# Kernel tuning notes

Hardware: AMD Instinct MI355X
Metric: run time of the kernel (lower is better)

## Reference

```python
import jax, jax.numpy as jnp
import numpy as np

NL = 8  # number of wavenet cells


def _causal_dil_conv(x, w, b, dil):
    # x: (B, Cin, T), w: (Cout, Cin, K) -> (B, Cout, T), left-padded (causal)
    pad = (w.shape[-1] - 1) * dil
    y = jax.lax.conv_general_dilated(
        x, w, window_strides=(1,), padding=[(pad, 0)],
        rhs_dilation=(dil,), dimension_numbers=('NCH', 'OIH', 'NCH'))
    return y + b[None, :, None]


def setup_inputs() -> dict:
    key = jax.random.key(0)
    ks = jax.random.split(key, 12)
    T, B, d_lag, d_cov, d, K = 2048, 16, 1, 7, 256, 2
    s = 0.05
    return {
        'x_lag': jax.random.normal(ks[0], (T, B, d_lag), jnp.float32),
        'x_cov': jax.random.normal(ks[1], (T, B, d_cov), jnp.float32),
        'up_W': jax.random.normal(ks[2], (d_lag + d_cov, d), jnp.float32) * s,
        'up_b': jax.random.normal(ks[3], (d,), jnp.float32) * s,
        'dil_w': jax.random.normal(ks[4], (NL, 2 * d, d, K), jnp.float32) * s,
        'dil_b': jax.random.normal(ks[5], (NL, 2 * d), jnp.float32) * s,
        'skip_w': jax.random.normal(ks[6], (NL, 2 * d, d, 1), jnp.float32) * s,
        'skip_b': jax.random.normal(ks[7], (NL, 2 * d), jnp.float32) * s,
        'loc_W': jax.random.normal(ks[8], (d, 1), jnp.float32) * s,
        'loc_b': jax.random.normal(ks[9], (1,), jnp.float32) * s,
        'proj_W': jax.random.normal(ks[10], (1, 1), jnp.float32) * s,
        'proj_b': jax.random.normal(ks[11], (1,), jnp.float32) * s,
        'd_outputseqlen': 96,
    }


def reference(x_lag, x_cov, up_W, up_b, dil_w, dil_b, skip_w, skip_b,
              loc_W, loc_b, proj_W, proj_b, d_outputseqlen):
    T = x_lag.shape[0]
    h = jnp.concatenate([x_lag, x_cov[:T]], axis=-1)          # (T,B,d_lag+d_cov)
    h = h @ up_W + up_b                                        # (T,B,d)
    h = jnp.transpose(h, (1, 2, 0))                            # (B,d,T)
    skip = jnp.zeros_like(h)
    for i in range(NL):
        z = _causal_dil_conv(h, dil_w[i], dil_b[i], 2 ** i)    # (B,2d,T)
        f, g = jnp.split(z, 2, axis=1)
        gated = jnp.tanh(f) * jax.nn.sigmoid(g)                # (B,d,T)
        z2 = _causal_dil_conv(gated, skip_w[i], skip_b[i], 1)  # (B,2d,T)
        h_next, skip_next = jnp.split(z2, 2, axis=1)
        h = h + h_next
        skip = skip + skip_next
    out = jnp.transpose(skip[:, :, -d_outputseqlen:], (2, 0, 1))  # (L,B,d)
    loc = out @ loc_W + loc_b                                     # (L,B,1)
    y = jnp.transpose(loc, (1, 0, 2))[..., None]                  # (B,L,1,1)
    return y @ proj_W + proj_b                                    # (B,L,1,c_out)
```

## Files before the change

### kernel.cpp

```cpp
#include <hip/hip_runtime.h>
#include <math.h>
#include <stdint.h>

#define T_TOTAL 2048
#define NB 16
#define D 256
#define T0 1696
#define TBUF 352
#define TSKIP 1952
#define LOUT 96

typedef __bf16 bf16x8 __attribute__((ext_vector_type(8)));
typedef __bf16 bf16x4v __attribute__((ext_vector_type(4)));
typedef float f32x4 __attribute__((ext_vector_type(4)));

__device__ __forceinline__ void gload_lds16(const void* src, void* lds_dst) {
    auto g = (const __attribute__((address_space(1))) void*)(uintptr_t)src;
    auto l = (__attribute__((address_space(3))) void*)(uintptr_t)(
                 (uint32_t)(uintptr_t)lds_dst);
    __builtin_amdgcn_global_load_lds(g, l, 16, 0, 0);
}

__device__ __forceinline__ void decode_tile(int id, int gridx, int& rt, int& ct) {
    int k = id & 7;
    int j = id >> 3;
    int rpx = gridx >> 6;
    rt = k * rpx + (j >> 3);
    ct = j & 7;
}

__global__ __launch_bounds__(256) void prep_up(
    const float* __restrict__ dil_w, const float* __restrict__ skip_w,
    const float* __restrict__ x_lag, const float* __restrict__ x_cov,
    const float* __restrict__ up_W, const float* __restrict__ up_b,
    const float* __restrict__ loc_W,
    __bf16* __restrict__ wT, __bf16* __restrict__ w2,
    float* __restrict__ hf, __bf16* __restrict__ hb,
    float* __restrict__ vWp)
{
    const int g0 = blockIdx.x * 256 + threadIdx.x;
    const int NT = 2048 * 256;

    for (int u = g0; u < 8 * 512 * 32; u += NT) {
        int j = u & 31;
        int cog = u >> 5;
        const float* src = dil_w + ((size_t)cog << 9) + (j << 4);
        float4 a = *(const float4*)(src);
        float4 b = *(const float4*)(src + 4);
        float4 c = *(const float4*)(src + 8);
        float4 d = *(const float4*)(src + 12);
        bf16x8 t0 = {(__bf16)a.x, (__bf16)a.z, (__bf16)b.x, (__bf16)b.z,
                     (__bf16)c.x, (__bf16)c.z, (__bf16)d.x, (__bf16)d.z};
        bf16x8 t1 = {(__bf16)a.y, (__bf16)a.w, (__bf16)b.y, (__bf16)b.w,
                     (__bf16)c.y, (__bf16)c.w, (__bf16)d.y, (__bf16)d.w};
        *(bf16x8*)(wT + ((size_t)cog << 9) + (j << 3)) = t0;
        *(bf16x8*)(wT + ((size_t)cog << 9) + 256 + (j << 3)) = t1;
    }
    for (int u = g0; u < 8 * 256 * 32; u += NT) {
        int row = u >> 5, j = u & 31;
        int ly = row >> 8, co = row & 255;
        const float* src = skip_w + (((size_t)(ly << 9) + co) << 8) + (j << 3);
        float4 a = *(const float4*)(src);
        float4 b = *(const float4*)(src + 4);
        bf16x8 v = {(__bf16)a.x, (__bf16)a.y, (__bf16)a.z, (__bf16)a.w,
                    (__bf16)b.x, (__bf16)b.y, (__bf16)b.z, (__bf16)b.w};
        *(bf16x8*)(w2 + ((size_t)row << 8) + (j << 3)) = v;
    }
    for (int u = g0; u < TBUF * NB * D; u += NT) {
        int row = u >> 8, c = u & 255;
        int tt = row >> 4, b = row & 15, t = T0 + tt;
        float acc = up_b[c] + x_lag[t * NB + b] * up_W[c];
        const float* cov = &x_cov[(t * NB + b) * 7];
        #pragma unroll
        for (int j = 0; j < 7; ++j)
            acc += cov[j] * up_W[(j + 1) * D + c];
        hf[u] = acc;
        hb[u] = (__bf16)acc;
    }
    for (int u = g0; u < 16384; u += NT) {
        int part = u >> 11;
        int r = u & 2047;
        int ly = r >> 8, ci = r & 255;
        const float* sw = skip_w + (((size_t)(ly << 9) + 256 + (part << 5)) << 8) + ci;
        float acc = 0.f;
        #pragma unroll 8
        for (int c = 0; c < 32; ++c)
            acc += sw[(size_t)c << 8] * loc_W[(part << 5) + c];
        vWp[u] = acc;
    }
}

__global__ __launch_bounds__(512, 4) void gate_n32(
    const __bf16* __restrict__ hb, __bf16* __restrict__ gated,
    const __bf16* __restrict__ wTl, const float* __restrict__ gbias,
    __bf16* __restrict__ gsv, int do_save,
    int tb, int dil, int M)
{
    __shared__ __align__(16) unsigned char lds[32768];
    int rt, ct;
    decode_tile(blockIdx.x, gridDim.x, rt, ct);
    const int m0 = rt << 6;
    if (m0 >= M) return;
    const int cb = ct << 5;
    const int tid = threadIdx.x;
    const int lane = tid & 63, wid = tid >> 6;
    const int wm = wid >> 1, wn = wid & 1;
    const int l15 = lane & 15, l4 = lane >> 4;
    const int arow = (wid << 3) + (lane >> 3);
    const int ach = lane & 7;
    const int aswz = (ach ^ (arow & 7)) << 3;
    const int bwid = wid & 3, bhalf = wid >> 2;
    const int brow = (bwid << 3) + (lane >> 3);
    const int bswz = (ach ^ (brow & 7)) << 3;
    const int roff1 = (tb - T0) * 16;
    const int roff0 = roff1 - dil * 16;

    f32x4 accf = {}, accg = {};

    auto stage = [&](int t, int buf) {
        const int k0 = t << 6;
        const int ci0 = k0 & 255;
        const int roff = (t < 4) ? roff0 : roff1;
        unsigned char* base = lds + buf * 16384;
        int m = m0 + arow; if (m >= M) m = M - 1;
        gload_lds16(hb + (size_t)(m + roff) * 256 + ci0 + aswz,
                    base + (wid << 10));
        gload_lds16(wTl + (size_t)(cb + bhalf * 256 + brow) * 512 + k0 + bswz,
                    base + 8192 + (bhalf << 12) + (bwid << 10));
    };

    stage(0, 0);
    for (int t = 0; t < 8; ++t) {
        const int buf = t & 1;
        if (t < 7) {
            stage(t + 1, buf ^ 1);
            asm volatile("s_waitcnt vmcnt(2)" ::: "memory");
        } else {
            asm volatile("s_waitcnt vmcnt(0)" ::: "memory");
        }
        __builtin_amdgcn_s_barrier();
        const unsigned char* base = lds + buf * 16384;
        __builtin_amdgcn_s_setprio(1);
        #pragma unroll
        for (int ks = 0; ks < 2; ++ks) {
            const int kb = (ks << 6) + (l4 << 4);
            int r = (wm << 4) + l15;
            bf16x8 av = *(const bf16x8*)(base + r * 128 + (kb ^ ((r & 7) << 4)));
            int n = (wn << 4) + l15;
            int o = n * 128 + (kb ^ ((n & 7) << 4));
            bf16x8 bfv = *(const bf16x8*)(base + 8192 + o);
            bf16x8 bgv = *(const bf16x8*)(base + 12288 + o);
            accf = __builtin_amdgcn_mfma_f32_16x16x32_bf16(av, bfv, accf, 0, 0, 0);
            accg = __builtin_amdgcn_mfma_f32_16x16x32_bf16(av, bgv, accg, 0, 0, 0);
        }
        __builtin_amdgcn_s_setprio(0);
        __builtin_amdgcn_s_barrier();
    }

    {
        const int ms0 = (TSKIP - tb) * 16;
        const int soff = (tb - TSKIP) * 16;
        int c = cb + (wn << 4) + l15;
        float bfb = gbias[c], bgb = gbias[c + 256];
        #pragma unroll
        for (int r = 0; r < 4; ++r) {
            int m = m0 + (wm << 4) + (l4 << 2) + r;
            if (m < M) {
                float fv = accf[r] + bfb;
                float gv = accg[r] + bgb;
                float th = 2.0f / (1.0f + __expf(-2.0f * fv)) - 1.0f;
                float sg = 1.0f / (1.0f + __expf(-gv));
                __bf16 val = (__bf16)(th * sg);
                gated[(size_t)m * 256 + c] = val;
                if (do_save && m >= ms0)
                    gsv[(size_t)(m + soff) * 256 + c] = val;
            }
        }
    }
}

__global__ __launch_bounds__(512, 4) void skip_h(
    const __bf16* __restrict__ gated, const __bf16* __restrict__ w2l,
    float* __restrict__ hf, __bf16* __restrict__ hb,
    const float* __restrict__ sbias, int tb, int M)
{
    __shared__ __align__(16) unsigned char lds[24576];
    int rt, ct;
    decode_tile(blockIdx.x, gridDim.x, rt, ct);
    const int m0 = rt << 6;
    if (m0 >= M) return;
    const int cb = ct << 5;
    const int tid = threadIdx.x;
    const int lane = tid & 63, wid = tid >> 6;
    const int wm = wid >> 1, wn = wid & 1;
    const int l15 = lane & 15, l4 = lane >> 4;
    const int arow = (wid << 3) + (lane >> 3);
    const int ach = lane & 7;
    const int aswz = (ach ^ (arow & 7)) << 3;
    const int brow = (wid << 3) + (lane >> 3);
    const int bswz = (ach ^ (brow & 7)) << 3;
    const int roff1 = (tb - T0) * 16;

    f32x4 acch = {};

    auto stage = [&](int t, int buf) {
        const int k0 = t << 6;
        unsigned char* base = lds + buf * 12288;
        int m = m0 + arow; if (m >= M) m = M - 1;
        gload_lds16(gated + (size_t)m * 256 + k0 + aswz,
                    base + (wid << 10));
        if (wid < 4)
            gload_lds16(w2l + (size_t)(cb + brow) * 256 + k0 + bswz,
                        base + 8192 + (wid << 10));
    };

    stage(0, 0);
    for (int t = 0; t < 4; ++t) {
        const int buf = t & 1;
        if (t < 3) {
            stage(t + 1, buf ^ 1);
            if (wid < 4) { asm volatile("s_waitcnt vmcnt(2)" ::: "memory"); }
            else         { asm volatile("s_waitcnt vmcnt(1)" ::: "memory"); }
        } else {
            asm volatile("s_waitcnt vmcnt(0)" ::: "memory");
        }
        __builtin_amdgcn_s_barrier();
        const unsigned char* base = lds + buf * 12288;
        __builtin_amdgcn_s_setprio(1);
        #pragma unroll
        for (int ks = 0; ks < 2; ++ks) {
            const int kb = (ks << 6) + (l4 << 4);
            int r = (wm << 4) + l15;
            bf16x8 av = *(const bf16x8*)(base + r * 128 + (kb ^ ((r & 7) << 4)));
            int n = (wn << 4) + l15;
            int o = n * 128 + (kb ^ ((n & 7) << 4));
            bf16x8 bhv = *(const bf16x8*)(base + 8192 + o);
            acch = __builtin_amdgcn_mfma_f32_16x16x32_bf16(av, bhv, acch, 0, 0, 0);
        }
        __builtin_amdgcn_s_setprio(0);
        __builtin_amdgcn_s_barrier();
    }

    {
        int c = cb + (wn << 4) + l15;
        float bhb = sbias[c];
        #pragma unroll
        for (int r = 0; r < 4; ++r) {
            int m = m0 + (wm << 4) + (l4 << 2) + r;
            if (m < M) {
                size_t hi = (size_t)(m + roff1) * 256 + c;
                float hv = hf[hi] + acch[r] + bhb;
                hf[hi] = hv;
                hb[hi] = (__bf16)hv;
            }
        }
    }
}

__global__ __launch_bounds__(256) void final_v2(
    const __bf16* __restrict__ gsave, const __bf16* __restrict__ gated,
    const float* __restrict__ vWp, const float* __restrict__ skip_b,
    const float* __restrict__ loc_W, const float* __restrict__ loc_b,
    const float* __restrict__ proj_W, const float* __restrict__ proj_b,
    float* __restrict__ out)
{
    int tid = threadIdx.x;
    int wid = tid >> 6, lane = tid & 63;
    int o = blockIdx.x * 4 + wid;
    float acc = 0.f;
    #pragma unroll
    for (int ly = 0; ly < 8; ++ly) {
        const __bf16* g = (ly < 7) ? gsave + (((size_t)ly * 1536 + o) << 8)
                                   : gated + ((size_t)o << 8);
        bf16x4v gv = *(const bf16x4v*)(g + (lane << 2));
        float4 vw = {0.f, 0.f, 0.f, 0.f};
        #pragma unroll
        for (int p = 0; p < 8; ++p) {
            float4 vp = *(const float4*)(vWp + (p << 11) + (ly << 8) + (lane << 2));
            vw.x += vp.x; vw.y += vp.y; vw.z += vp.z; vw.w += vp.w;
        }
        acc += (float)gv[0] * vw.x + (float)gv[1] * vw.y
             + (float)gv[2] * vw.z + (float)gv[3] * vw.w;
    }
    #pragma unroll
    for (int j = 0; j < 32; ++j) {
        int idx = lane + (j << 6);
        int ly = idx >> 8, c = idx & 255;
        acc += skip_b[(ly << 9) + 256 + c] * loc_W[c];
    }
    #pragma unroll
    for (int off = 32; off; off >>= 1) acc += __shfl_down(acc, off);
    if (lane == 0) {
        int l = o >> 4, b = o & 15;
        out[b * LOUT + l] = (acc + loc_b[0]) * proj_W[0] + proj_b[0];
    }
}

extern "C" void kernel_launch(void* const* d_in, const int* in_sizes, int n_in,
                              void* d_out, int out_size, void* d_ws, size_t ws_size,
                              hipStream_t stream)
{
    const float* x_lag  = (const float*)d_in[0];
    const float* x_cov  = (const float*)d_in[1];
    const float* up_W   = (const float*)d_in[2];
    const float* up_b   = (const float*)d_in[3];
    const float* dil_w  = (const float*)d_in[4];
    const float* dil_b  = (const float*)d_in[5];
    const float* skip_w = (const float*)d_in[6];
    const float* skip_b = (const float*)d_in[7];
    const float* loc_W  = (const float*)d_in[8];
    const float* loc_b  = (const float*)d_in[9];
    const float* proj_W = (const float*)d_in[10];
    const float* proj_b = (const float*)d_in[11];
    float* out = (float*)d_out;

    unsigned char* ws = (unsigned char*)d_ws;
    float*  hf    = (float*)ws;
    __bf16* hb    = (__bf16*)(ws + 5767168);
    __bf16* gated = (__bf16*)(ws + 8650752);
    __bf16* gsave = (__bf16*)(ws + 11534336);
    __bf16* wT    = (__bf16*)(ws + 17039360);
    __bf16* w2    = (__bf16*)(ws + 21233664);
    float*  vWp   = (float*)(ws + 22282240);

    hipLaunchKernelGGL(prep_up, dim3(2048), dim3(256), 0, stream,
                       dil_w, skip_w, x_lag, x_cov, up_W, up_b, loc_W,
                       wT, w2, hf, hb, vWp);

    for (int i = 0; i < 8; ++i) {
        int dil = 1 << i;
        int tb  = T0 + 2 * dil;
        int M   = (T_TOTAL - tb) * NB;
        int mt  = (M + 63) >> 6;
        int mtp = (mt + 7) & ~7;
        const __bf16* wTl = wT + (size_t)i * 512 * 512;
        const __bf16* w2l = w2 + (size_t)i * 256 * 256;
        const float* gb = dil_b + (size_t)i * 512;
        const float* sb = skip_b + (size_t)i * 512;

        hipLaunchKernelGGL(gate_n32, dim3(mtp * 8), dim3(512), 0, stream,
                           hb, gated, wTl, gb,
                           gsave + (size_t)i * 1536 * 256, i < 7 ? 1 : 0,
                           tb, dil, M);
        if (i < 7)
            hipLaunchKernelGGL(skip_h, dim3(mtp * 8), dim3(512), 0, stream,
                               gated, w2l, hf, hb, sb, tb, M);
    }
    hipLaunchKernelGGL(final_v2, dim3(LOUT * NB / 4), dim3(256), 0, stream,
                       gsave, gated, vWp, skip_b, loc_W, loc_b, proj_W, proj_b,
                       out);
}
```

Measured before the change: 123.6 us.

## Fold skip conv into next layer's gate GEMM via precomputed product weights

Precomputes V = W_dil(i+1) · W_skip_h(i) so each layer's gate GEMM reads the previous layer's gated activations directly, using K=1024 instead of waiting for the h update. This lets the skip/h update of layer i run concurrently with the gate of layer i+1 in one fused launch. Double-buffered h and gated buffers avoid read/write hazards, and per-layer tail contributions are accumulated incrementally instead of saved and reduced at the end. It costs a doubled gate GEMM K dimension, an extra prep GEMM, and extra bf16 rounding of the composed weights.

```diff
diff --git a/kernel.cpp b/kernel.cpp
--- a/kernel.cpp
+++ b/kernel.cpp
@@ -34,7 +34,7 @@
     const float* __restrict__ x_lag, const float* __restrict__ x_cov,
     const float* __restrict__ up_W, const float* __restrict__ up_b,
     const float* __restrict__ loc_W,
-    __bf16* __restrict__ wT, __bf16* __restrict__ w2,
+    __bf16* __restrict__ wT, __bf16* __restrict__ w2, __bf16* __restrict__ w2T,
     float* __restrict__ hf, __bf16* __restrict__ hb,
     float* __restrict__ vWp)
 {
@@ -56,7 +56,7 @@
         *(bf16x8*)(wT + ((size_t)cog << 9) + (j << 3)) = t0;
         *(bf16x8*)(wT + ((size_t)cog << 9) + 256 + (j << 3)) = t1;
     }
-    for (int u = g0; u < 8 * 256 * 32; u += NT) {
+    for (int u = g0; u < 7 * 256 * 32; u += NT) {
         int row = u >> 5, j = u & 31;
         int ly = row >> 8, co = row & 255;
         const float* src = skip_w + (((size_t)(ly << 9) + co) << 8) + (j << 3);
@@ -65,6 +65,9 @@
         bf16x8 v = {(__bf16)a.x, (__bf16)a.y, (__bf16)a.z, (__bf16)a.w,
                     (__bf16)b.x, (__bf16)b.y, (__bf16)b.z, (__bf16)b.w};
         *(bf16x8*)(w2 + ((size_t)row << 8) + (j << 3)) = v;
+        __bf16* wt = w2T + ((size_t)ly << 16) + (j << 3) * 256 + co;
+        #pragma unroll
+        for (int e = 0; e < 8; ++e) wt[e << 8] = v[e];
     }
     for (int u = g0; u < TBUF * NB * D; u += NT) {
         int row = u >> 8, c = u & 255;
@@ -90,10 +93,95 @@
     }
 }
 
+__global__ __launch_bounds__(512, 4) void prep_v(
+    const __bf16* __restrict__ wT, const __bf16* __restrict__ w2T,
+    const float* __restrict__ dil_b, const float* __restrict__ skip_b,
+    __bf16* __restrict__ V, float* __restrict__ cbias)
+{
+    __shared__ __align__(16) unsigned char lds[24576];
+    const int id = blockIdx.x;
+    const int tid = threadIdx.x;
+    const int lane = tid & 63, wid = tid >> 6;
+    if (id >= 896) {
+        int n = (id - 896) * 8 + wid;
+        int i1 = n >> 9, n0 = n & 511;
+        const __bf16* wrow = wT + (((size_t)(i1 + 1) << 18) + ((size_t)n0 << 9));
+        const float* sb = skip_b + (i1 << 9);
+        float s = 0.f;
+        #pragma unroll
+        for (int e = 0; e < 8; ++e) {
+            int k = (lane << 3) + e;
+            s += sb[k & 255] * (float)wrow[k];
+        }
+        #pragma unroll
+        for (int off = 32; off; off >>= 1) s += __shfl_down(s, off);
+        if (lane == 0)
+            cbias[(i1 << 9) + n0] = dil_b[((i1 + 1) << 9) + n0] + s;
+        return;
+    }
+    const int i1 = id / 128;
+    const int r = id - i1 * 128;
+    const int a = r >> 6;
+    const int rt = (r & 63) >> 3, ct = r & 7;
+    const int n0t = rt << 6;
+    const int cb = ct << 5;
+    const __bf16* Awt = wT + (((size_t)(i1 + 1) << 18)) + (a << 8);
+    const __bf16* Bw = w2T + ((size_t)i1 << 16);
+    const int wm = wid >> 1, wn = wid & 1;
+    const int l15 = lane & 15, l4 = lane >> 4;
+    const int arow = (wid << 3) + (lane >> 3);
+    const int ach = lane & 7;
+    const int aswz = (ach ^ (arow & 7)) << 3;
+    const int brow = (wid << 3) + (lane >> 3);
+    const int bswz = (ach ^ (brow & 7)) << 3;
+
+    f32x4 acc = {};
+    auto stage = [&](int t, int buf) {
+        const int k0 = t << 6;
+        unsigned char* base = lds + buf * 12288;
+        gload_lds16(Awt + (size_t)(n0t + arow) * 512 + k0 + aswz,
+                    base + (wid << 10));
+        if (wid < 4)
+            gload_lds16(Bw + (size_t)(cb + brow) * 256 + k0 + bswz,
+                        base + 8192 + (wid << 10));
+    };
+    stage(0, 0);
+    for (int t = 0; t < 4; ++t) {
+        const int buf = t & 1;
+        if (t < 3) {
+            stage(t + 1, buf ^ 1);
+            if (wid < 4) { asm volatile("s_waitcnt vmcnt(2)" ::: "memory"); }
+            else         { asm volatile("s_waitcnt vmcnt(1)" ::: "memory"); }
+        } else {
+            asm volatile("s_waitcnt vmcnt(0)" ::: "memory");
+        }
+        __builtin_amdgcn_s_barrier();
+        const unsigned char* base = lds + buf * 12288;
+        #pragma unroll
+        for (int ks = 0; ks < 2; ++ks) {
+            const int kb = (ks << 6) + (l4 << 4);
+            int rr = (wm << 4) + l15;
+            bf16x8 av = *(const bf16x8*)(base + rr * 128 + (kb ^ ((rr & 7) << 4)));
+            int nn = (wn << 4) + l15;
+            int o = nn * 128 + (kb ^ ((nn & 7) << 4));
+            bf16x8 bv = *(const bf16x8*)(base + 8192 + o);
+            acc = __builtin_amdgcn_mfma_f32_16x16x32_bf16(av, bv, acc, 0, 0, 0);
+        }
+        __builtin_amdgcn_s_barrier();
+    }
+    {
+        int c = cb + (wn << 4) + l15;
+        #pragma unroll
+        for (int rr = 0; rr < 4; ++rr) {
+            int n = n0t + (wm << 4) + (l4 << 2) + rr;
+            V[((size_t)i1 << 18) + (size_t)n * 512 + (a << 8) + c] = (__bf16)acc[rr];
+        }
+    }
+}
+
 __global__ __launch_bounds__(512, 4) void gate_n32(
     const __bf16* __restrict__ hb, __bf16* __restrict__ gated,
     const __bf16* __restrict__ wTl, const float* __restrict__ gbias,
-    __bf16* __restrict__ gsv, int do_save,
     int tb, int dil, int M)
 {
     __shared__ __align__(16) unsigned char lds[32768];
@@ -116,7 +204,6 @@
     const int roff0 = roff1 - dil * 16;
 
     f32x4 accf = {}, accg = {};
-
     auto stage = [&](int t, int buf) {
         const int k0 = t << 6;
         const int ci0 = k0 & 255;
@@ -128,7 +215,6 @@
         gload_lds16(wTl + (size_t)(cb + bhalf * 256 + brow) * 512 + k0 + bswz,
                     base + 8192 + (bhalf << 12) + (bwid << 10));
     };
-
     stage(0, 0);
     for (int t = 0; t < 8; ++t) {
         const int buf = t & 1;
@@ -156,10 +242,7 @@
         __builtin_amdgcn_s_setprio(0);
         __builtin_amdgcn_s_barrier();
     }
-
     {
-        const int ms0 = (TSKIP - tb) * 16;
-        const int soff = (tb - TSKIP) * 16;
         int c = cb + (wn << 4) + l15;
         float bfb = gbias[c], bgb = gbias[c + 256];
         #pragma unroll
@@ -170,96 +253,197 @@
                 float gv = accg[r] + bgb;
                 float th = 2.0f / (1.0f + __expf(-2.0f * fv)) - 1.0f;
                 float sg = 1.0f / (1.0f + __expf(-gv));
-                __bf16 val = (__bf16)(th * sg);
-                gated[(size_t)m * 256 + c] = val;
-                if (do_save && m >= ms0)
-                    gsv[(size_t)(m + soff) * 256 + c] = val;
-            }
-        }
-    }
-}
-
-__global__ __launch_bounds__(512, 4) void skip_h(
-    const __bf16* __restrict__ gated, const __bf16* __restrict__ w2l,
-    float* __restrict__ hf, __bf16* __restrict__ hb,
-    const float* __restrict__ sbias, int tb, int M)
+                gated[(size_t)m * 256 + c] = (__bf16)(th * sg);
+            }
+        }
+    }
+}
+
+__global__ __launch_bounds__(512, 4) void fused_layer(
+    const __bf16* __restrict__ hb_r, const __bf16* __restrict__ gb_r,
+    __bf16* __restrict__ gb_w,
+    const __bf16* __restrict__ wTl, const __bf16* __restrict__ Vl,
+    const float* __restrict__ cbias_l,
+    int tb_g, int dil_g, int Mg, int ngate,
+    const __bf16* __restrict__ w2l, const float* __restrict__ sbias,
+    float* __restrict__ hf, __bf16* __restrict__ hb_w,
+    int tb_s, int Ms, int nskip,
+    const float* __restrict__ vWl, float* __restrict__ accb,
+    int goff_t, int first_tail)
 {
-    __shared__ __align__(16) unsigned char lds[24576];
-    int rt, ct;
-    decode_tile(blockIdx.x, gridDim.x, rt, ct);
-    const int m0 = rt << 6;
-    if (m0 >= M) return;
-    const int cb = ct << 5;
+    __shared__ __align__(16) unsigned char lds[32768];
+    const int id = blockIdx.x;
     const int tid = threadIdx.x;
     const int lane = tid & 63, wid = tid >> 6;
     const int wm = wid >> 1, wn = wid & 1;
     const int l15 = lane & 15, l4 = lane >> 4;
-    const int arow = (wid << 3) + (lane >> 3);
     const int ach = lane & 7;
-    const int aswz = (ach ^ (arow & 7)) << 3;
-    const int brow = (wid << 3) + (lane >> 3);
-    const int bswz = (ach ^ (brow & 7)) << 3;
-    const int roff1 = (tb - T0) * 16;
-
-    f32x4 acch = {};
-
-    auto stage = [&](int t, int buf) {
-        const int k0 = t << 6;
-        unsigned char* base = lds + buf * 12288;
-        int m = m0 + arow; if (m >= M) m = M - 1;
-        gload_lds16(gated + (size_t)m * 256 + k0 + aswz,
-                    base + (wid << 10));
-        if (wid < 4)
-            gload_lds16(w2l + (size_t)(cb + brow) * 256 + k0 + bswz,
-                        base + 8192 + (wid << 10));
-    };
-
-    stage(0, 0);
-    for (int t = 0; t < 4; ++t) {
-        const int buf = t & 1;
-        if (t < 3) {
-            stage(t + 1, buf ^ 1);
-            if (wid < 4) { asm volatile("s_waitcnt vmcnt(2)" ::: "memory"); }
-            else         { asm volatile("s_waitcnt vmcnt(1)" ::: "memory"); }
-        } else {
-            asm volatile("s_waitcnt vmcnt(0)" ::: "memory");
-        }
-        __builtin_amdgcn_s_barrier();
-        const unsigned char* base = lds + buf * 12288;
-        __builtin_amdgcn_s_setprio(1);
-        #pragma unroll
-        for (int ks = 0; ks < 2; ++ks) {
-            const int kb = (ks << 6) + (l4 << 4);
-            int r = (wm << 4) + l15;
-            bf16x8 av = *(const bf16x8*)(base + r * 128 + (kb ^ ((r & 7) << 4)));
-            int n = (wn << 4) + l15;
-            int o = n * 128 + (kb ^ ((n & 7) << 4));
-            bf16x8 bhv = *(const bf16x8*)(base + 8192 + o);
-            acch = __builtin_amdgcn_mfma_f32_16x16x32_bf16(av, bhv, acch, 0, 0, 0);
-        }
-        __builtin_amdgcn_s_setprio(0);
-        __builtin_amdgcn_s_barrier();
-    }
-
-    {
-        int c = cb + (wn << 4) + l15;
-        float bhb = sbias[c];
-        #pragma unroll
-        for (int r = 0; r < 4; ++r) {
-            int m = m0 + (wm << 4) + (l4 << 2) + r;
-            if (m < M) {
-                size_t hi = (size_t)(m + roff1) * 256 + c;
-                float hv = hf[hi] + acch[r] + bhb;
-                hf[hi] = hv;
-                hb[hi] = (__bf16)hv;
-            }
-        }
-    }
-}
-
-__global__ __launch_bounds__(256) void final_v2(
-    const __bf16* __restrict__ gsave, const __bf16* __restrict__ gated,
-    const float* __restrict__ vWp, const float* __restrict__ skip_b,
+
+    if (id < ngate) {
+        int rt, ct;
+        decode_tile(id, ngate, rt, ct);
+        const int m0 = rt << 6;
+        if (m0 >= Mg) return;
+        const int cb = ct << 5;
+        const int arow = (wid << 3) + (lane >> 3);
+        const int aswz = (ach ^ (arow & 7)) << 3;
+        const int bwid = wid & 3, bhalf = wid >> 2;
+        const int brow = (bwid << 3) + (lane >> 3);
+        const int bswz = (ach ^ (brow & 7)) << 3;
+        const int roff1 = (tb_g - T0) * 16;
+        const int roff0 = roff1 - dil_g * 16;
+        const int goff1 = dil_g * 16;
+
+        f32x4 accf = {}, accg = {};
+        auto stage = [&](int t, int buf) {
+            const int k0 = t << 6;
+            unsigned char* base = lds + buf * 16384;
+            int m = m0 + arow; if (m >= Mg) m = Mg - 1;
+            if (t < 8) {
+                const int ci0 = k0 & 255;
+                const int roff = (t < 4) ? roff0 : roff1;
+                gload_lds16(hb_r + (size_t)(m + roff) * 256 + ci0 + aswz,
+                            base + (wid << 10));
+                gload_lds16(wTl + (size_t)(cb + bhalf * 256 + brow) * 512 + k0 + bswz,
+                            base + 8192 + (bhalf << 12) + (bwid << 10));
+            } else {
+                const int c0 = k0 & 255;
+                const int go = (t < 12) ? 0 : goff1;
+                gload_lds16(gb_r + (size_t)(m + go) * 256 + c0 + aswz,
+                            base + (wid << 10));
+                gload_lds16(Vl + (size_t)(cb + bhalf * 256 + brow) * 512 + (k0 - 512) + bswz,
+                            base + 8192 + (bhalf << 12) + (bwid << 10));
+            }
+        };
+        stage(0, 0);
+        for (int t = 0; t < 16; ++t) {
+            const int buf = t & 1;
+            if (t < 15) {
+                stage(t + 1, buf ^ 1);
+                asm volatile("s_waitcnt vmcnt(2)" ::: "memory");
+            } else {
+                asm volatile("s_waitcnt vmcnt(0)" ::: "memory");
+            }
+            __builtin_amdgcn_s_barrier();
+            const unsigned char* base = lds + buf * 16384;
+            __builtin_amdgcn_s_setprio(1);
+            #pragma unroll
+            for (int ks = 0; ks < 2; ++ks) {
+                const int kb = (ks << 6) + (l4 << 4);
+                int r = (wm << 4) + l15;
+                bf16x8 av = *(const bf16x8*)(base + r * 128 + (kb ^ ((r & 7) << 4)));
+                int n = (wn << 4) + l15;
+                int o = n * 128 + (kb ^ ((n & 7) << 4));
+                bf16x8 bfv = *(const bf16x8*)(base + 8192 + o);
+                bf16x8 bgv = *(const bf16x8*)(base + 12288 + o);
+                accf = __builtin_amdgcn_mfma_f32_16x16x32_bf16(av, bfv, accf, 0, 0, 0);
+                accg = __builtin_amdgcn_mfma_f32_16x16x32_bf16(av, bgv, accg, 0, 0, 0);
+            }
+            __builtin_amdgcn_s_setprio(0);
+            __builtin_amdgcn_s_barrier();
+        }
+        {
+            int c = cb + (wn << 4) + l15;
+            float bfb = cbias_l[c], bgb = cbias_l[c + 256];
+            #pragma unroll
+            for (int r = 0; r < 4; ++r) {
+                int m = m0 + (wm << 4) + (l4 << 2) + r;
+                if (m < Mg) {
+                    float fv = accf[r] + bfb;
+                    float gv = accg[r] + bgb;
+                    float th = 2.0f / (1.0f + __expf(-2.0f * fv)) - 1.0f;
+                    float sg = 1.0f / (1.0f + __expf(-gv));
+                    gb_w[(size_t)m * 256 + c] = (__bf16)(th * sg);
+                }
+            }
+        }
+    } else if (id < ngate + nskip) {
+        int rt, ct;
+        decode_tile(id - ngate, nskip, rt, ct);
+        const int m0 = rt << 6;
+        if (m0 >= Ms) return;
+        const int cb = ct << 5;
+        const int arow = (wid << 3) + (lane >> 3);
+        const int aswz = (ach ^ (arow & 7)) << 3;
+        const int brow = (wid << 3) + (lane >> 3);
+        const int bswz = (ach ^ (brow & 7)) << 3;
+        const int roff1 = (tb_s - T0) * 16;
+
+        f32x4 acch = {};
+        auto stage = [&](int t, int buf) {
+            const int k0 = t << 6;
+            unsigned char* base = lds + buf * 12288;
+            int m = m0 + arow; if (m >= Ms) m = Ms - 1;
+            gload_lds16(gb_r + (size_t)m * 256 + k0 + aswz,
+                        base + (wid << 10));
+            if (wid < 4)
+                gload_lds16(w2l + (size_t)(cb + brow) * 256 + k0 + bswz,
+                            base + 8192 + (wid << 10));
+        };
+        stage(0, 0);
+        for (int t = 0; t < 4; ++t) {
+            const int buf = t & 1;
+            if (t < 3) {
+                stage(t + 1, buf ^ 1);
+                if (wid < 4) { asm volatile("s_waitcnt vmcnt(2)" ::: "memory"); }
+                else         { asm volatile("s_waitcnt vmcnt(1)" ::: "memory"); }
+            } else {
+                asm volatile("s_waitcnt vmcnt(0)" ::: "memory");
+            }
+            __builtin_amdgcn_s_barrier();
+            const unsigned char* base = lds + buf * 12288;
+            __builtin_amdgcn_s_setprio(1);
+            #pragma unroll
+            for (int ks = 0; ks < 2; ++ks) {
+                const int kb = (ks << 6) + (l4 << 4);
+                int r = (wm << 4) + l15;
+                bf16x8 av = *(const bf16x8*)(base + r * 128 + (kb ^ ((r & 7) << 4)));
+                int n = (wn << 4) + l15;
+                int o = n * 128 + (kb ^ ((n & 7) << 4));
+                bf16x8 bhv = *(const bf16x8*)(base + 8192 + o);
+                acch = __builtin_amdgcn_mfma_f32_16x16x32_bf16(av, bhv, acch, 0, 0, 0);
+            }
+            __builtin_amdgcn_s_setprio(0);
+            __builtin_amdgcn_s_barrier();
+        }
+        {
+            int c = cb + (wn << 4) + l15;
+            float bhb = sbias[c];
+            #pragma unroll
+            for (int r = 0; r < 4; ++r) {
+                int m = m0 + (wm << 4) + (l4 << 2) + r;
+                if (m < Ms) {
+                    size_t hi = (size_t)(m + roff1) * 256 + c;
+                    float hv = hf[hi] + acch[r] + bhb;
+                    hf[hi] = hv;
+                    hb_w[hi] = (__bf16)hv;
+                }
+            }
+        }
+    } else {
+        int o = (id - ngate - nskip) * 8 + wid;
+        const __bf16* g = gb_r + (size_t)(o + goff_t) * 256;
+        bf16x4v gv = *(const bf16x4v*)(g + (lane << 2));
+        float4 vw = {0.f, 0.f, 0.f, 0.f};
+        #pragma unroll
+        for (int p = 0; p < 8; ++p) {
+            float4 vp = *(const float4*)(vWl + (p << 11) + (lane << 2));
+            vw.x += vp.x; vw.y += vp.y; vw.z += vp.z; vw.w += vp.w;
+        }
+        float s = (float)gv[0] * vw.x + (float)gv[1] * vw.y
+                + (float)gv[2] * vw.z + (float)gv[3] * vw.w;
+        #pragma unroll
+        for (int off = 32; off; off >>= 1) s += __shfl_down(s, off);
+        if (lane == 0) {
+            if (first_tail) accb[o] = s;
+            else accb[o] += s;
+        }
+    }
+}
+
+__global__ __launch_bounds__(256) void final_v3(
+    const __bf16* __restrict__ gb7, const float* __restrict__ vWp,
+    const float* __restrict__ accb, const float* __restrict__ skip_b,
     const float* __restrict__ loc_W, const float* __restrict__ loc_b,
     const float* __restrict__ proj_W, const float* __restrict__ proj_b,
     float* __restrict__ out)
@@ -267,21 +451,15 @@
     int tid = threadIdx.x;
     int wid = tid >> 6, lane = tid & 63;
     int o = blockIdx.x * 4 + wid;
-    float acc = 0.f;
+    bf16x4v gv = *(const bf16x4v*)(gb7 + ((size_t)o << 8) + (lane << 2));
+    float4 vw = {0.f, 0.f, 0.f, 0.f};
     #pragma unroll
-    for (int ly = 0; ly < 8; ++ly) {
-        const __bf16* g = (ly < 7) ? gsave + (((size_t)ly * 1536 + o) << 8)
-                                   : gated + ((size_t)o << 8);
-        bf16x4v gv = *(const bf16x4v*)(g + (lane << 2));
-        float4 vw = {0.f, 0.f, 0.f, 0.f};
-        #pragma unroll
-        for (int p = 0; p < 8; ++p) {
-            float4 vp = *(const float4*)(vWp + (p << 11) + (ly << 8) + (lane << 2));
-            vw.x += vp.x; vw.y += vp.y; vw.z += vp.z; vw.w += vp.w;
-        }
-        acc += (float)gv[0] * vw.x + (float)gv[1] * vw.y
-             + (float)gv[2] * vw.z + (float)gv[3] * vw.w;
-    }
+    for (int p = 0; p < 8; ++p) {
+        float4 vp = *(const float4*)(vWp + (p << 11) + (7 << 8) + (lane << 2));
+        vw.x += vp.x; vw.y += vp.y; vw.z += vp.z; vw.w += vp.w;
+    }
+    float acc = (float)gv[0] * vw.x + (float)gv[1] * vw.y
+              + (float)gv[2] * vw.z + (float)gv[3] * vw.w;
     #pragma unroll
     for (int j = 0; j < 32; ++j) {
         int idx = lane + (j << 6);
@@ -292,7 +470,7 @@
     for (int off = 32; off; off >>= 1) acc += __shfl_down(acc, off);
     if (lane == 0) {
         int l = o >> 4, b = o & 15;
-        out[b * LOUT + l] = (acc + loc_b[0]) * proj_W[0] + proj_b[0];
+        out[b * LOUT + l] = (acc + accb[o] + loc_b[0]) * proj_W[0] + proj_b[0];
     }
 }
 
@@ -316,37 +494,51 @@
 
     unsigned char* ws = (unsigned char*)d_ws;
     float*  hf    = (float*)ws;
-    __bf16* hb    = (__bf16*)(ws + 5767168);
-    __bf16* gated = (__bf16*)(ws + 8650752);
-    __bf16* gsave = (__bf16*)(ws + 11534336);
-    __bf16* wT    = (__bf16*)(ws + 17039360);
-    __bf16* w2    = (__bf16*)(ws + 21233664);
-    float*  vWp   = (float*)(ws + 22282240);
+    __bf16* hbuf[2] = { (__bf16*)(ws + 5767168),
+                        (__bf16*)(ws + 8650752) };
+    __bf16* gbuf[2] = { (__bf16*)(ws + 11534336),
+                        (__bf16*)(ws + 14417920) };
+    __bf16* wT    = (__bf16*)(ws + 17301504);
+    __bf16* V     = (__bf16*)(ws + 21495808);
+    __bf16* w2    = (__bf16*)(ws + 25165824);
+    __bf16* w2T   = (__bf16*)(ws + 26083328);
+    float*  vWp   = (float*)(ws + 27000832);
+    float*  cbias = (float*)(ws + 27066368);
+    float*  accb  = (float*)(ws + 27080704);
 
     hipLaunchKernelGGL(prep_up, dim3(2048), dim3(256), 0, stream,
                        dil_w, skip_w, x_lag, x_cov, up_W, up_b, loc_W,
-                       wT, w2, hf, hb, vWp);
-
-    for (int i = 0; i < 8; ++i) {
+                       wT, w2, w2T, hf, hbuf[0], vWp);
+    hipLaunchKernelGGL(prep_v, dim3(1344), dim3(512), 0, stream,
+                       wT, w2T, dil_b, skip_b, V, cbias);
+
+    {
+        int tb = T0 + 2, M = (T_TOTAL - tb) * NB;
+        int mtp = (((M + 63) >> 6) + 7) & ~7;
+        hipLaunchKernelGGL(gate_n32, dim3(mtp * 8), dim3(512), 0, stream,
+                           hbuf[0], gbuf[0], wT, dil_b, tb, 1, M);
+    }
+    for (int i = 1; i < 8; ++i) {
         int dil = 1 << i;
-        int tb  = T0 + 2 * dil;
-        int M   = (T_TOTAL - tb) * NB;
-        int mt  = (M + 63) >> 6;
-        int mtp = (mt + 7) & ~7;
-        const __bf16* wTl = wT + (size_t)i * 512 * 512;
-        const __bf16* w2l = w2 + (size_t)i * 256 * 256;
-        const float* gb = dil_b + (size_t)i * 512;
-        const float* sb = skip_b + (size_t)i * 512;
-
-        hipLaunchKernelGGL(gate_n32, dim3(mtp * 8), dim3(512), 0, stream,
-                           hb, gated, wTl, gb,
-                           gsave + (size_t)i * 1536 * 256, i < 7 ? 1 : 0,
-                           tb, dil, M);
-        if (i < 7)
-            hipLaunchKernelGGL(skip_h, dim3(mtp * 8), dim3(512), 0, stream,
-                               gated, w2l, hf, hb, sb, tb, M);
-    }
-    hipLaunchKernelGGL(final_v2, dim3(LOUT * NB / 4), dim3(256), 0, stream,
-                       gsave, gated, vWp, skip_b, loc_W, loc_b, proj_W, proj_b,
+        int tb_g = T0 + 2 * dil;
+        int Mg = (T_TOTAL - tb_g) * NB;
+        int ngate = ((((Mg + 63) >> 6) + 7) & ~7) * 8;
+        int s = i - 1;
+        int tb_s = T0 + 2 * (1 << s);
+        int Ms = (T_TOTAL - tb_s) * NB;
+        int nskip = (i < 7) ? ((((Ms + 63) >> 6) + 7) & ~7) * 8 : 0;
+        hipLaunchKernelGGL(fused_layer, dim3(ngate + nskip + 192), dim3(512), 0,
+                           stream,
+                           hbuf[s & 1], gbuf[s & 1], gbuf[i & 1],
+                           wT + ((size_t)i << 18), V + ((size_t)s << 18),
+                           cbias + (s << 9),
+                           tb_g, dil, Mg, ngate,
+                           w2 + ((size_t)s << 16), skip_b + (s << 9),
+                           hf, hbuf[i & 1], tb_s, Ms, nskip,
+                           vWp + (s << 8), accb,
+                           (TSKIP - tb_s) * 16, i == 1 ? 1 : 0);
+    }
+    hipLaunchKernelGGL(final_v3, dim3(LOUT * NB / 4), dim3(256), 0, stream,
+                       gbuf[1], vWp, accb, skip_b, loc_W, loc_b, proj_W, proj_b,
                        out);
 }
```

After: 127.8 us. 1.03x slower.
